# Performance work log

Hardware: AMD Instinct MI355X
Metric: run time of the kernel (lower is better)

## Reference

```python
import jax, jax.numpy as jnp
import numpy as np

N = 20000      # nodes
E1 = 100000    # topo (2d) edges
E2 = 100000    # distance edges
HID = 128      # hidden_size
N2D = 128      # node_embed_size_2d
E2D = 64       # edge_embed_size_2d
EF = 128       # edge_feat_size
ET = 32        # edge_type_size
NRBF = 64
CUT = 6.0


def rbf_expand(d):
    # Gaussian radial basis with cosine cutoff envelope, d: [E]
    centers = jnp.linspace(0.0, CUT, NRBF)
    width = CUT / NRBF
    env = 0.5 * (jnp.cos(jnp.pi * jnp.clip(d / CUT, 0.0, 1.0)) + 1.0)
    return jnp.exp(-((d[:, None] - centers) ** 2) / (2.0 * width * width)) * env[:, None]


def setup_inputs() -> dict:
    key = jax.random.key(0)
    ks = jax.random.split(key, 20)
    s = 0.02
    return {
        "H": jax.random.normal(ks[0], (N, HID), jnp.float32),
        "V": jax.random.normal(ks[1], (N, HID, 3), jnp.float32),
        "Z": jax.random.normal(ks[2], (N, 3), jnp.float32) * 3.0,
        "layer_i": 0,
        "H_2d": jax.random.normal(ks[3], (N, N2D), jnp.float32),
        "mask_2d": jnp.ones((N,), bool),
        "E2d_idx": jax.random.randint(ks[4], (2, E1), 0, N),
        "E2d_feat": jax.random.normal(ks[5], (E2D, E1), jnp.float32),
        "Z_3d": jax.random.normal(ks[6], (N, 3), jnp.float32) * 3.0,
        "mask_3d": jnp.ones((N,), bool),
        "Edist_idx": jax.random.randint(ks[7], (2, E2), 0, N),
        "Edist_val": jax.random.uniform(ks[8], (E2,), jnp.float32) * CUT,
        "virtual_node_embed": jax.random.normal(ks[9], (1, N2D), jnp.float32),
        "edge_type_embed": jax.random.normal(ks[10], (3, ET), jnp.float32),
        "W_rbf": jax.random.normal(ks[11], (EF, NRBF), jnp.float32) * s,
        "W_e2d": jax.random.normal(ks[12], (EF, E2D), jnp.float32) * s,
        "W_i": jax.random.normal(ks[13], (HID, HID + N2D), jnp.float32) * s,
        "W_phi1": jax.random.normal(ks[14], (HID, HID + EF + ET), jnp.float32) * s,
        "b_phi1": jnp.zeros((HID,), jnp.float32),
        "W_phi2": jax.random.normal(ks[15], (3 * HID, HID), jnp.float32) * s,
        "b_phi2": jnp.zeros((3 * HID,), jnp.float32),
        "W_msg": jax.random.normal(ks[16], (3 * HID, NRBF), jnp.float32) * s,
        "b_msg": jnp.zeros((3 * HID,), jnp.float32),
    }


def reference(H, V, Z, layer_i, H_2d, mask_2d, E2d_idx, E2d_feat, Z_3d, mask_3d,
              Edist_idx, Edist_val, virtual_node_embed, edge_type_embed,
              W_rbf, W_e2d, W_i, W_phi1, b_phi1, W_phi2, b_phi2, W_msg, b_msg):
    n = H.shape[0]
    # mask_3d is all-True in this fixture => n_cond_3d == n (static shapes)
    nodes_real = jnp.concatenate([H, H_2d], axis=-1)                       # [n, h1+h2]
    virt = jnp.broadcast_to(virtual_node_embed, (n, virtual_node_embed.shape[1]))
    nodes_virt = jnp.concatenate([H, virt], axis=-1)                        # [n, h1+h2]
    nodes = jnp.concatenate([nodes_real, nodes_virt], axis=0) @ W_i.T      # [2n, h1]
    v = jnp.concatenate([V, jnp.zeros_like(V)], axis=0)                     # [2n, h1, 3]
    z = jnp.concatenate([Z, Z_3d], axis=0)                                  # [2n, 3]

    row_3d = jnp.arange(n)
    col_3d = jnp.arange(n) + n
    E3d = jnp.stack([jnp.concatenate([row_3d, col_3d]),
                     jnp.concatenate([col_3d, row_3d])], axis=0)            # [2, 2n]
    edges = jnp.concatenate([E2d_idx, E3d, Edist_idx], axis=-1)             # [2, E]
    e1, e3, e2 = E2d_idx.shape[1], E3d.shape[1], Edist_idx.shape[1]
    edge_type = jnp.concatenate([jnp.zeros((e1,), jnp.int32),
                                 jnp.ones((e3,), jnp.int32),
                                 jnp.full((e2,), 2, jnp.int32)])
    et = edge_type_embed[edge_type]                                         # [E, ET]
    attr2d = E2d_feat.T @ W_e2d.T                                           # [e1, EF]
    attr3d = jnp.zeros((e3, W_e2d.shape[0]), jnp.float32)                   # [e3, EF]
    attrd = rbf_expand(Edist_val) @ W_rbf.T                                 # [e2, EF]
    edge_attr = jnp.concatenate(
        [jnp.concatenate([attr2d, attr3d, attrd], axis=0), et], axis=-1)    # [E, EF+ET]

    # AdapterLayer: PaiNN-style equivariant message passing
    row, col = edges[0], edges[1]
    rel = z[row] - z[col]                                                   # [E, 3]
    dist = jnp.sqrt(jnp.sum(rel * rel, axis=-1) + 1e-8)                     # [E]
    unit = rel / dist[:, None]
    phi_in = jnp.concatenate([nodes[col], edge_attr], axis=-1)
    phi = jax.nn.silu(phi_in @ W_phi1.T + b_phi1) @ W_phi2.T + b_phi2       # [E, 3h]
    wd = rbf_expand(dist) @ W_msg.T + b_msg                                 # [E, 3h]
    m = phi * wd
    h = nodes.shape[1]
    s_msg, v_gate, r_gate = m[:, :h], m[:, h:2 * h], m[:, 2 * h:]
    dv = v[col] * v_gate[:, :, None] + unit[:, None, :] * r_gate[:, :, None]  # [E, h, 3]
    nn2 = nodes.shape[0]
    H_add = jax.ops.segment_sum(s_msg, row, num_segments=nn2)[:n]
    V_add = jax.ops.segment_sum(dv, row, num_segments=nn2)[:n]

    # eval-mode clamp
    H_add = jnp.clip(H_add, -100.0, 100.0)
    V_add = jnp.clip(V_add, -100.0, 100.0)

    mask_dist = jnp.zeros((n,), bool).at[Edist_idx[0]].set(True).at[Edist_idx[1]].set(True)
    update_mask = mask_2d | mask_3d | mask_dist
    H_add = jnp.where(update_mask[:, None], H_add, 0.0)
    V_add = jnp.where(update_mask[:, None, None], V_add, 0.0)
    return H_add, V_add
```

## Files before the change

kernel.cpp:

```cpp
#include <hip/hip_runtime.h>
#include <hip/hip_bf16.h>

#define NN   20000
#define E1N  100000
#define E2N  100000
#define NEFF 220000
#define TILE 64
#define NBLK ((NEFF + TILE - 1) / TILE)
#define NPAD (NBLK * TILE)
#define RBF_STEP   0.09523809523809523f
#define RBF_INV2W2 56.88888888888889f

typedef short  bf16x8 __attribute__((ext_vector_type(8)));
typedef float  f32x4  __attribute__((ext_vector_type(4)));

__device__ __forceinline__ float4 ld4(const float* p) {
    return *reinterpret_cast<const float4*>(p);
}
__device__ __forceinline__ ushort f2bf(float x) {
    __hip_bfloat16 h = __float2bfloat16(x);
    return *reinterpret_cast<ushort*>(&h);
}
__device__ __forceinline__ float bf2f(ushort u) {
    return __uint_as_float(((unsigned)u) << 16);
}
__device__ __forceinline__ float env_of(float d) {
    float x = fminf(fmaxf(d * (1.0f / 6.0f), 0.0f), 1.0f);
    return 0.5f * (__cosf(3.14159265358979f * x) + 1.0f);
}
__device__ __forceinline__ float clip100(float x) {
    return fminf(fmaxf(x, -100.f), 100.f);
}

__device__ __forceinline__ int edge_row(int eid, const int* __restrict__ E2d_idx,
                                        const int* __restrict__ Edist_idx) {
    if (eid < E1N) return E2d_idx[eid];
    if (eid < E1N + NN) return eid - E1N;
    return Edist_idx[eid - E1N - NN];
}

__global__ __launch_bounds__(256) void hist_kernel(
    const int* __restrict__ E2d_idx, const int* __restrict__ Edist_idx,
    int* __restrict__ hist) {
    int g = blockIdx.x * 256 + threadIdx.x;
    if (g < NEFF) atomicAdd(&hist[edge_row(g, E2d_idx, Edist_idx)], 1);
}

__global__ __launch_bounds__(256) void scan_kernel(
    const int* __restrict__ hist, int* __restrict__ start, int* __restrict__ cursor) {
    __shared__ int wsum[4];
    const int t = threadIdx.x;
    const int base = t * 80;
    int s = 0;
    for (int j = 0; j < 80; ++j) {
        int idx = base + j;
        if (idx < NN) s += hist[idx];
    }
    const int lane = t & 63, w = t >> 6;
    int v = s;
    for (int off = 1; off < 64; off <<= 1) {
        int x = __shfl_up(v, off, 64);
        if (lane >= off) v += x;
    }
    if (lane == 63) wsum[w] = v;
    __syncthreads();
    int woff = 0;
    for (int i = 0; i < w; ++i) woff += wsum[i];
    int run = woff + v - s;
    for (int j = 0; j < 80; ++j) {
        int idx = base + j;
        if (idx < NN) {
            start[idx] = run;
            cursor[idx] = run;
            run += hist[idx];
        }
    }
    if (t == 255) start[NN] = run;
}

__global__ __launch_bounds__(256) void scatter_kernel(
    const int* __restrict__ E2d_idx, const int* __restrict__ Edist_idx,
    int* __restrict__ cursor, int* __restrict__ order) {
    int g = blockIdx.x * 256 + threadIdx.x;
    if (g < NEFF) {
        int r = edge_row(g, E2d_idx, Edist_idx);
        int pos = atomicAdd(&cursor[r], 1);
        order[pos] = g;
    }
}

__global__ __launch_bounds__(256) void meta_kernel(
    const int* __restrict__ order, const int* __restrict__ E2d_idx,
    const int* __restrict__ Edist_idx, const float* __restrict__ Edist_val,
    const float* __restrict__ Z, const float* __restrict__ Z3d,
    int4* __restrict__ metaI, float4* __restrict__ metaF,
    float4* __restrict__ metaU) {
    int g = blockIdx.x * 256 + threadIdx.x;
    if (g >= NPAD) return;
    int eid = (g < NEFF) ? order[g] : -1;
    int row, col, ty, e2 = 0; float dval = 0.f;
    if (eid < 0)             { ty = 1; row = -1; col = 0; }
    else if (eid < E1N)      { ty = 0; row = E2d_idx[eid]; col = E2d_idx[E1N + eid]; e2 = eid; }
    else if (eid < E1N + NN) { ty = 1; int jj = eid - E1N; row = jj; col = jj + NN; }
    else { ty = 2; int g2 = eid - E1N - NN;
           row = Edist_idx[g2]; col = Edist_idx[E2N + g2]; dval = Edist_val[g2]; }
    int rs = (row < 0) ? 0 : row;
    float prx = Z[rs * 3], pry = Z[rs * 3 + 1], prz = Z[rs * 3 + 2];
    float pcx, pcy, pcz;
    if (col < NN) { pcx = Z[col * 3]; pcy = Z[col * 3 + 1]; pcz = Z[col * 3 + 2]; }
    else { int c = col - NN; pcx = Z3d[c * 3]; pcy = Z3d[c * 3 + 1]; pcz = Z3d[c * 3 + 2]; }
    float dx = prx - pcx, dy = pry - pcy, dz = prz - pcz;
    float dist = sqrtf(dx * dx + dy * dy + dz * dz + 1e-8f);
    float inv = 1.0f / dist;
    int vcol = (col < NN) ? col : -1;
    metaI[g] = make_int4(col, row, ty, e2);
    metaF[g] = make_float4(dist, dval, env_of(dist), env_of(dval));
    metaU[g] = (row >= 0)
        ? make_float4(dx * inv, dy * inv, dz * inv, __int_as_float(vcol))
        : make_float4(0.f, 0.f, 0.f, __int_as_float(-1));
}

__global__ __launch_bounds__(256) void prep_kernel(
    const float* __restrict__ W_phi1, const float* __restrict__ b_phi1,
    const float* __restrict__ W_e2d, const float* __restrict__ W_rbf,
    const float* __restrict__ W_phi2, const float* __restrict__ W_msg,
    const float* __restrict__ et, const float* __restrict__ W_i,
    ushort* __restrict__ W1c, ushort* __restrict__ W2b,
    ushort* __restrict__ Wmb, float* __restrict__ b_type,
    ushort* __restrict__ Wib) {
    int g = blockIdx.x * 256 + threadIdx.x;
    if (g < 32768) {
        int n = g >> 8, k = g & 255;
        float v;
        if (k < 128) v = W_phi1[n * 288 + k];
        else {
            int kk = k - 128;
            const float* Wsel = (kk < 64) ? W_e2d : W_rbf;
            int j = kk & 63;
            float s = 0.f;
            for (int a = 0; a < 128; ++a) s += W_phi1[n * 288 + 128 + a] * Wsel[a * 64 + j];
            v = s;
        }
        W1c[n * 256 + k] = f2bf(v);
    } else if (g < 81920) {
        int q = g - 32768; W2b[q] = f2bf(W_phi2[q]);
    } else if (g < 106496) {
        int q = g - 81920; Wmb[q] = f2bf(W_msg[q]);
    } else if (g < 106880) {
        int q = g - 106496; int ty = q >> 7, n = q & 127;
        float s = b_phi1[n];
        for (int a = 0; a < 32; ++a) s += W_phi1[n * 288 + 256 + a] * et[ty * 32 + a];
        b_type[q] = s;
    } else if (g < 139648) {
        int q = g - 106880; Wib[q] = f2bf(W_i[q]);
    }
}

__global__ __launch_bounds__(256) void featT_kernel(
    const float* __restrict__ feat, ushort* __restrict__ featTb) {
    __shared__ float tile[64][65];
    const int t = threadIdx.x;
    const int cbase = blockIdx.x * 64;
    for (int i = t; i < 64 * 64; i += 256) {
        int k = i >> 6, e = i & 63;
        tile[k][e] = (cbase + e < E1N) ? feat[(size_t)k * E1N + cbase + e] : 0.f;
    }
    __syncthreads();
    for (int i = t; i < 64 * 64; i += 256) {
        int e = i >> 6, k = i & 63;
        if (cbase + e < E1N) featTb[(size_t)(cbase + e) * 64 + k] = f2bf(tile[k][e]);
    }
}

__global__ __launch_bounds__(256, 2) void nodes_mfma_kernel(
    const float* __restrict__ H, const float* __restrict__ H2d,
    const float* __restrict__ virt, const ushort* __restrict__ Wib,
    ushort* __restrict__ nodesb) {
    __shared__ ushort A[64][264];
    __shared__ ushort WB[128][132];

    const int t = threadIdx.x;
    const int gbase = blockIdx.x * 64;

    for (int i = t; i < 64 * 64; i += 256) {
        int e = i >> 6, q = i & 63;
        int row = gbase + e;
        float4 v;
        if (q < 32)          v = ld4(H + (size_t)((row < NN) ? row : row - NN) * 128 + q * 4);
        else if (row < NN)   v = ld4(H2d + (size_t)row * 128 + (q - 32) * 4);
        else                 v = ld4(virt + (q - 32) * 4);
        ushort tmp[4] = {f2bf(v.x), f2bf(v.y), f2bf(v.z), f2bf(v.w)};
        *reinterpret_cast<uint2*>(&A[e][q * 4]) = *reinterpret_cast<const uint2*>(tmp);
    }
    for (int i = t; i < 128 * 16; i += 256) {
        int n = i >> 4, q = i & 15;
        *reinterpret_cast<uint4*>(&WB[n][q * 8]) =
            *reinterpret_cast<const uint4*>(Wib + (size_t)n * 256 + q * 8);
    }
    __syncthreads();

    const int w  = t >> 6, lane = t & 63;
    const int mh = w >> 1, nh = w & 1;
    const int lr = lane >> 4, lc = lane & 15;
    const int ar0 = mh * 32 + lc;

    f32x4 acc[2][4];
#pragma unroll
    for (int mt = 0; mt < 2; ++mt)
#pragma unroll
        for (int nt = 0; nt < 4; ++nt) acc[mt][nt] = (f32x4){0.f, 0.f, 0.f, 0.f};
#pragma unroll
    for (int ks = 0; ks < 4; ++ks) {
        bf16x8 a0 = *reinterpret_cast<const bf16x8*>(&A[ar0][ks * 32 + lr * 8]);
        bf16x8 a1 = *reinterpret_cast<const bf16x8*>(&A[ar0 + 16][ks * 32 + lr * 8]);
#pragma unroll
        for (int nt = 0; nt < 4; ++nt) {
            int n = nh * 64 + nt * 16 + lc;
            bf16x8 b = *reinterpret_cast<const bf16x8*>(&WB[n][ks * 32 + lr * 8]);
            acc[0][nt] = __builtin_amdgcn_mfma_f32_16x16x32_bf16(a0, b, acc[0][nt], 0, 0, 0);
            acc[1][nt] = __builtin_amdgcn_mfma_f32_16x16x32_bf16(a1, b, acc[1][nt], 0, 0, 0);
        }
    }
    __syncthreads();
    for (int i = t; i < 128 * 16; i += 256) {
        int n = i >> 4, q = i & 15;
        *reinterpret_cast<uint4*>(&WB[n][q * 8]) =
            *reinterpret_cast<const uint4*>(Wib + (size_t)n * 256 + 128 + q * 8);
    }
    __syncthreads();
#pragma unroll
    for (int ks = 4; ks < 8; ++ks) {
        bf16x8 a0 = *reinterpret_cast<const bf16x8*>(&A[ar0][ks * 32 + lr * 8]);
        bf16x8 a1 = *reinterpret_cast<const bf16x8*>(&A[ar0 + 16][ks * 32 + lr * 8]);
#pragma unroll
        for (int nt = 0; nt < 4; ++nt) {
            int n = nh * 64 + nt * 16 + lc;
            bf16x8 b = *reinterpret_cast<const bf16x8*>(&WB[n][(ks - 4) * 32 + lr * 8]);
            acc[0][nt] = __builtin_amdgcn_mfma_f32_16x16x32_bf16(a0, b, acc[0][nt], 0, 0, 0);
            acc[1][nt] = __builtin_amdgcn_mfma_f32_16x16x32_bf16(a1, b, acc[1][nt], 0, 0, 0);
        }
    }
#pragma unroll
    for (int mt = 0; mt < 2; ++mt)
#pragma unroll
        for (int nt = 0; nt < 4; ++nt)
#pragma unroll
            for (int r = 0; r < 4; ++r) {
                int e  = mh * 32 + mt * 16 + lr * 4 + r;
                int ch = nh * 64 + nt * 16 + lc;
                nodesb[(size_t)(gbase + e) * 128 + ch] = f2bf(acc[mt][nt][r]);
            }
}

__global__ __launch_bounds__(256, 3) void edge1_kernel(
    const ushort* __restrict__ nodesb, const ushort* __restrict__ featTb,
    const ushort* __restrict__ W1c, const ushort* __restrict__ W2b,
    const ushort* __restrict__ Wmb, const float* __restrict__ b_type,
    const float* __restrict__ b_phi2, const float* __restrict__ b_msg,
    const int4* __restrict__ metaI, const float4* __restrict__ metaF,
    ushort* __restrict__ payloadM) {

    __shared__ ushort sm[26752];
    ushort* WB   = sm;
    ushort* HM   = sm + 16896;
    float*  s_bt = (float*)(sm + 25600);
    int*    s_col= (int*)(sm + 26368);
    int*    s_ty = (int*)(sm + 26496);
    int*    s_e2 = (int*)(sm + 26624);

    const int t = threadIdx.x;
    const int gbase = blockIdx.x * TILE;

    if (t < TILE) {
        int4 mi = metaI[gbase + t];
        s_col[t] = mi.x; s_ty[t] = mi.z; s_e2[t] = mi.w;
    }
    for (int i = t; i < 384; i += 256) s_bt[i] = b_type[i];
    for (int i = t; i < 128 * 16; i += 256) {
        int n = i >> 4, q = i & 15;
        *reinterpret_cast<uint4*>(WB + n * 132 + q * 8) =
            *reinterpret_cast<const uint4*>(W1c + (size_t)n * 256 + q * 8);
    }
    __syncthreads();

    const int w  = t >> 6, lane = t & 63;
    const int mh = w >> 1, nh = w & 1;
    const int lr = lane >> 4, lc = lane & 15;
    const int ar0 = mh * 32 + lc;

    const int colA = s_col[ar0],      colB = s_col[ar0 + 16];
    const int tyA  = s_ty[ar0],       tyB  = s_ty[ar0 + 16];
    const int e2A  = s_e2[ar0],       e2B  = s_e2[ar0 + 16];
    const float4 mfA = metaF[gbase + ar0];
    const float4 mfB = metaF[gbase + ar0 + 16];

    bf16x8 a0[8], a1[8];
    const bf16x8 zz = {0, 0, 0, 0, 0, 0, 0, 0};
#pragma unroll
    for (int ks = 0; ks < 4; ++ks) {
        a0[ks] = *reinterpret_cast<const bf16x8*>(nodesb + (size_t)colA * 128 + ks * 32 + lr * 8);
        a1[ks] = *reinterpret_cast<const bf16x8*>(nodesb + (size_t)colB * 128 + ks * 32 + lr * 8);
    }
#pragma unroll
    for (int ks = 4; ks < 6; ++ks) {
        bf16x8 fA = *reinterpret_cast<const bf16x8*>(featTb + (size_t)e2A * 64 + (ks - 4) * 32 + lr * 8);
        bf16x8 fB = *reinterpret_cast<const bf16x8*>(featTb + (size_t)e2B * 64 + (ks - 4) * 32 + lr * 8);
        a0[ks] = (tyA == 0) ? fA : zz;
        a1[ks] = (tyB == 0) ? fB : zz;
    }
#pragma unroll
    for (int ks = 6; ks < 8; ++ks) {
#pragma unroll
        for (int j = 0; j < 8; ++j) {
            float cc = (float)((ks - 6) * 32 + lr * 8 + j) * RBF_STEP;
            float tA = mfA.y - cc, tB = mfB.y - cc;
            ushort vA = f2bf(__expf(-tA * tA * RBF_INV2W2) * mfA.w);
            ushort vB = f2bf(__expf(-tB * tB * RBF_INV2W2) * mfB.w);
            a0[ks][j] = (tyA == 2) ? (short)vA : (short)0;
            a1[ks][j] = (tyB == 2) ? (short)vB : (short)0;
        }
    }
    bf16x8 ra0[2], ra1[2];
#pragma unroll
    for (int ks = 0; ks < 2; ++ks)
#pragma unroll
        for (int j = 0; j < 8; ++j) {
            float cc = (float)(ks * 32 + lr * 8 + j) * RBF_STEP;
            float tA = mfA.x - cc, tB = mfB.x - cc;
            ra0[ks][j] = (short)f2bf(__expf(-tA * tA * RBF_INV2W2) * mfA.z);
            ra1[ks][j] = (short)f2bf(__expf(-tB * tB * RBF_INV2W2) * mfB.z);
        }

    f32x4 acc[2][4];
#pragma unroll
    for (int mt = 0; mt < 2; ++mt)
#pragma unroll
        for (int nt = 0; nt < 4; ++nt) acc[mt][nt] = (f32x4){0.f, 0.f, 0.f, 0.f};
#pragma unroll
    for (int ks = 0; ks < 4; ++ks) {
#pragma unroll
        for (int nt = 0; nt < 4; ++nt) {
            int n = nh * 64 + nt * 16 + lc;
            bf16x8 b = *reinterpret_cast<const bf16x8*>(WB + n * 132 + ks * 32 + lr * 8);
            acc[0][nt] = __builtin_amdgcn_mfma_f32_16x16x32_bf16(a0[ks], b, acc[0][nt], 0, 0, 0);
            acc[1][nt] = __builtin_amdgcn_mfma_f32_16x16x32_bf16(a1[ks], b, acc[1][nt], 0, 0, 0);
        }
    }
    __syncthreads();
    for (int i = t; i < 128 * 16; i += 256) {
        int n = i >> 4, q = i & 15;
        *reinterpret_cast<uint4*>(WB + n * 132 + q * 8) =
            *reinterpret_cast<const uint4*>(W1c + (size_t)n * 256 + 128 + q * 8);
    }
    __syncthreads();
#pragma unroll
    for (int ks = 4; ks < 8; ++ks) {
#pragma unroll
        for (int nt = 0; nt < 4; ++nt) {
            int n = nh * 64 + nt * 16 + lc;
            bf16x8 b = *reinterpret_cast<const bf16x8*>(WB + n * 132 + (ks - 4) * 32 + lr * 8);
            acc[0][nt] = __builtin_amdgcn_mfma_f32_16x16x32_bf16(a0[ks], b, acc[0][nt], 0, 0, 0);
            acc[1][nt] = __builtin_amdgcn_mfma_f32_16x16x32_bf16(a1[ks], b, acc[1][nt], 0, 0, 0);
        }
    }
    __syncthreads();

#pragma unroll
    for (int mt = 0; mt < 2; ++mt)
#pragma unroll
        for (int nt = 0; nt < 4; ++nt)
#pragma unroll
            for (int r = 0; r < 4; ++r) {
                int e  = mh * 32 + mt * 16 + lr * 4 + r;
                int ch = nh * 64 + nt * 16 + lc;
                float x = acc[mt][nt][r] + s_bt[s_ty[e] * 128 + ch];
                HM[e * 136 + ch] = f2bf(x / (1.0f + __expf(-x)));
            }
    for (int i = t; i < 128 * 16; i += 256) {
        int n = i >> 4, q = i & 15;
        *reinterpret_cast<uint4*>(WB + n * 132 + q * 8) =
            *reinterpret_cast<const uint4*>(W2b + (size_t)n * 128 + q * 8);
    }
    __syncthreads();

    bf16x8 ha0[4], ha1[4];
#pragma unroll
    for (int ks = 0; ks < 4; ++ks) {
        ha0[ks] = *reinterpret_cast<const bf16x8*>(HM + ar0 * 136 + ks * 32 + lr * 8);
        ha1[ks] = *reinterpret_cast<const bf16x8*>(HM + (ar0 + 16) * 136 + ks * 32 + lr * 8);
    }

#pragma unroll
    for (int c = 0; c < 3; ++c) {
        f32x4 p[2][4], g[2][4];
#pragma unroll
        for (int mt = 0; mt < 2; ++mt)
#pragma unroll
            for (int nt = 0; nt < 4; ++nt) {
                p[mt][nt] = (f32x4){0.f, 0.f, 0.f, 0.f};
                g[mt][nt] = (f32x4){0.f, 0.f, 0.f, 0.f};
            }
#pragma unroll
        for (int ks = 0; ks < 4; ++ks) {
#pragma unroll
            for (int nt = 0; nt < 4; ++nt) {
                int n = nh * 64 + nt * 16 + lc;
                bf16x8 b = *reinterpret_cast<const bf16x8*>(WB + n * 132 + ks * 32 + lr * 8);
                p[0][nt] = __builtin_amdgcn_mfma_f32_16x16x32_bf16(ha0[ks], b, p[0][nt], 0, 0, 0);
                p[1][nt] = __builtin_amdgcn_mfma_f32_16x16x32_bf16(ha1[ks], b, p[1][nt], 0, 0, 0);
            }
        }
#pragma unroll
        for (int ks = 0; ks < 2; ++ks) {
#pragma unroll
            for (int nt = 0; nt < 4; ++nt) {
                int n = c * 128 + nh * 64 + nt * 16 + lc;
                bf16x8 b = *reinterpret_cast<const bf16x8*>(Wmb + (size_t)n * 64 + ks * 32 + lr * 8);
                g[0][nt] = __builtin_amdgcn_mfma_f32_16x16x32_bf16(ra0[ks], b, g[0][nt], 0, 0, 0);
                g[1][nt] = __builtin_amdgcn_mfma_f32_16x16x32_bf16(ra1[ks], b, g[1][nt], 0, 0, 0);
            }
        }
        __syncthreads();
#pragma unroll
        for (int mt = 0; mt < 2; ++mt)
#pragma unroll
            for (int nt = 0; nt < 4; ++nt) {
                int d  = nh * 64 + nt * 16 + lc;
                float b2 = b_phi2[c * 128 + d];
                float bm = b_msg[c * 128 + d];
#pragma unroll
                for (int r = 0; r < 4; ++r) {
                    int e = mh * 32 + mt * 16 + lr * 4 + r;
                    HM[e * 136 + d] = f2bf((p[mt][nt][r] + b2) * (g[mt][nt][r] + bm));
                }
            }
        if (c < 2) {
            for (int i = t; i < 128 * 16; i += 256) {
                int n = i >> 4, q = i & 15;
                *reinterpret_cast<uint4*>(WB + n * 132 + q * 8) =
                    *reinterpret_cast<const uint4*>(W2b + (size_t)((c + 1) * 128 + n) * 128 + q * 8);
            }
        }
        __syncthreads();
        for (int i = t; i < 2048; i += 256) {
            int e = i >> 5, q = i & 31;
            *reinterpret_cast<uint2*>(payloadM + (size_t)(gbase + e) * 384 + c * 128 + q * 4) =
                *reinterpret_cast<const uint2*>(HM + e * 136 + q * 4);
        }
    }
}

__global__ __launch_bounds__(256, 2) void edge0_kernel(
    const ushort* __restrict__ nodesb, const float* __restrict__ V,
    const float* __restrict__ Z, const float* __restrict__ Z3d,
    const int* __restrict__ E2d_idx, const float* __restrict__ E2d_feat,
    const int* __restrict__ Edist_idx, const float* __restrict__ Edist_val,
    const ushort* __restrict__ W1c, const ushort* __restrict__ W2b,
    const ushort* __restrict__ Wmb, const float* __restrict__ b_type,
    const float* __restrict__ b_phi2, const float* __restrict__ b_msg,
    float* __restrict__ Hout, float* __restrict__ Vout) {

    __shared__ ushort A1[TILE][264];
    __shared__ float  s_bt[3][128];
    __shared__ int    s_row[TILE], s_col[TILE], s_ty[TILE], s_e2[TILE], s_vcol[TILE];
    __shared__ float  s_dist[TILE], s_dval[TILE], s_env[TILE], s_env2[TILE];
    __shared__ float  s_unit[TILE][3];
    ushort (*hid)[136] = reinterpret_cast<ushort(*)[136]>(&A1[0][0]);

    const int t = threadIdx.x;
    const int gbase = blockIdx.x * TILE;
    if (t < TILE) {
        int gpos = gbase + t;
        int eid = (gpos < NEFF) ? gpos : -1;
        int row, col, ty, e2 = 0; float dval = 0.f;
        if (eid < 0)             { ty = 1; row = -1; col = 0; }
        else if (eid < E1N)      { ty = 0; row = E2d_idx[eid]; col = E2d_idx[E1N + eid]; e2 = eid; }
        else if (eid < E1N + NN) { ty = 1; int jj = eid - E1N; row = jj; col = jj + NN; }
        else { ty = 2; int g2 = eid - E1N - NN;
               row = Edist_idx[g2]; col = Edist_idx[E2N + g2]; dval = Edist_val[g2]; }
        int rs = (row < 0) ? 0 : row;
        float prx = Z[rs * 3], pry = Z[rs * 3 + 1], prz = Z[rs * 3 + 2];
        float pcx, pcy, pcz;
        if (col < NN) { pcx = Z[col * 3]; pcy = Z[col * 3 + 1]; pcz = Z[col * 3 + 2]; }
        else { int c = col - NN; pcx = Z3d[c * 3]; pcy = Z3d[c * 3 + 1]; pcz = Z3d[c * 3 + 2]; }
        float dx = prx - pcx, dy = pry - pcy, dz = prz - pcz;
        float dist = sqrtf(dx * dx + dy * dy + dz * dz + 1e-8f);
        float inv = 1.0f / dist;
        s_row[t] = row; s_col[t] = col; s_ty[t] = ty; s_e2[t] = e2;
        s_vcol[t] = (col < NN) ? col : -1;
        s_unit[t][0] = dx * inv; s_unit[t][1] = dy * inv; s_unit[t][2] = dz * inv;
        s_dist[t] = dist; s_dval[t] = dval;
        s_env[t] = env_of(dist); s_env2[t] = env_of(dval);
    }
    for (int i = t; i < 384; i += 256) ((float*)s_bt)[i] = b_type[i];
    __syncthreads();

    for (int i = t; i < TILE * 16; i += 256) {
        int e = i >> 4, q = i & 15;
        *reinterpret_cast<uint4*>(&A1[e][q * 8]) =
            *reinterpret_cast<const uint4*>(nodesb + (size_t)s_col[e] * 128 + q * 8);
    }
    for (int i = t; i < TILE * 128; i += 256) {
        int k = i >> 6, e = i & 63;
        int ty = s_ty[e];
        float v = 0.f;
        if (ty == 0) { if (k < 64) v = E2d_feat[(size_t)k * E1N + s_e2[e]]; }
        else if (ty == 2) {
            if (k >= 64) {
                float dd = s_dval[e] - (float)(k - 64) * RBF_STEP;
                v = __expf(-dd * dd * RBF_INV2W2) * s_env2[e];
            }
        }
        A1[e][128 + k] = f2bf(v);
    }
    __syncthreads();

    const int w  = t >> 6, lane = t & 63;
    const int mh = w >> 1, nh = w & 1;
    const int lr = lane >> 4, lc = lane & 15;
    const int ar0 = mh * 32 + lc;

    bf16x8 ra0[2], ra1[2];
    {
        float dA = s_dist[ar0],      eA = s_env[ar0];
        float dB = s_dist[ar0 + 16], eB = s_env[ar0 + 16];
#pragma unroll
        for (int ks = 0; ks < 2; ++ks)
#pragma unroll
            for (int j = 0; j < 8; ++j) {
                float c  = (float)(ks * 32 + lr * 8 + j) * RBF_STEP;
                float tA = dA - c, tB = dB - c;
                ra0[ks][j] = (short)f2bf(__expf(-tA * tA * RBF_INV2W2) * eA);
                ra1[ks][j] = (short)f2bf(__expf(-tB * tB * RBF_INV2W2) * eB);
            }
    }

    f32x4 acc[2][4];
#pragma unroll
    for (int mt = 0; mt < 2; ++mt)
#pragma unroll
        for (int nt = 0; nt < 4; ++nt) acc[mt][nt] = (f32x4){0.f, 0.f, 0.f, 0.f};
#pragma unroll
    for (int ks = 0; ks < 8; ++ks) {
        bf16x8 a0 = *reinterpret_cast<const bf16x8*>(&A1[ar0][ks * 32 + lr * 8]);
        bf16x8 a1 = *reinterpret_cast<const bf16x8*>(&A1[ar0 + 16][ks * 32 + lr * 8]);
#pragma unroll
        for (int nt = 0; nt < 4; ++nt) {
            int n = nh * 64 + nt * 16 + lc;
            bf16x8 b = *reinterpret_cast<const bf16x8*>(W1c + (size_t)n * 256 + ks * 32 + lr * 8);
            acc[0][nt] = __builtin_amdgcn_mfma_f32_16x16x32_bf16(a0, b, acc[0][nt], 0, 0, 0);
            acc[1][nt] = __builtin_amdgcn_mfma_f32_16x16x32_bf16(a1, b, acc[1][nt], 0, 0, 0);
        }
    }
    __syncthreads();
#pragma unroll
    for (int mt = 0; mt < 2; ++mt)
#pragma unroll
        for (int nt = 0; nt < 4; ++nt)
#pragma unroll
            for (int r = 0; r < 4; ++r) {
                int e  = mh * 32 + mt * 16 + lr * 4 + r;
                int ch = nh * 64 + nt * 16 + lc;
                float x = acc[mt][nt][r] + s_bt[s_ty[e]][ch];
                hid[e][ch] = f2bf(x / (1.0f + __expf(-x)));
            }
    __syncthreads();

    f32x4 vgr[2][4];
#pragma unroll
    for (int c = 0; c < 3; ++c) {
        f32x4 p[2][4], g[2][4];
#pragma unroll
        for (int mt = 0; mt < 2; ++mt)
#pragma unroll
            for (int nt = 0; nt < 4; ++nt) {
                p[mt][nt] = (f32x4){0.f, 0.f, 0.f, 0.f};
                g[mt][nt] = (f32x4){0.f, 0.f, 0.f, 0.f};
            }
#pragma unroll
        for (int ks = 0; ks < 4; ++ks) {
            bf16x8 a0 = *reinterpret_cast<const bf16x8*>(&hid[ar0][ks * 32 + lr * 8]);
            bf16x8 a1 = *reinterpret_cast<const bf16x8*>(&hid[ar0 + 16][ks * 32 + lr * 8]);
#pragma unroll
            for (int nt = 0; nt < 4; ++nt) {
                int n = c * 128 + nh * 64 + nt * 16 + lc;
                bf16x8 b = *reinterpret_cast<const bf16x8*>(W2b + (size_t)n * 128 + ks * 32 + lr * 8);
                p[0][nt] = __builtin_amdgcn_mfma_f32_16x16x32_bf16(a0, b, p[0][nt], 0, 0, 0);
                p[1][nt] = __builtin_amdgcn_mfma_f32_16x16x32_bf16(a1, b, p[1][nt], 0, 0, 0);
            }
        }
#pragma unroll
        for (int ks = 0; ks < 2; ++ks) {
#pragma unroll
            for (int nt = 0; nt < 4; ++nt) {
                int n = c * 128 + nh * 64 + nt * 16 + lc;
                bf16x8 b = *reinterpret_cast<const bf16x8*>(Wmb + (size_t)n * 64 + ks * 32 + lr * 8);
                g[0][nt] = __builtin_amdgcn_mfma_f32_16x16x32_bf16(ra0[ks], b, g[0][nt], 0, 0, 0);
                g[1][nt] = __builtin_amdgcn_mfma_f32_16x16x32_bf16(ra1[ks], b, g[1][nt], 0, 0, 0);
            }
        }
#pragma unroll
        for (int mt = 0; mt < 2; ++mt)
#pragma unroll
            for (int nt = 0; nt < 4; ++nt) {
                int d  = nh * 64 + nt * 16 + lc;
                float b2 = b_phi2[c * 128 + d];
                float bm = b_msg[c * 128 + d];
#pragma unroll
                for (int r = 0; r < 4; ++r) {
                    int e = mh * 32 + mt * 16 + lr * 4 + r;
                    float m = (p[mt][nt][r] + b2) * (g[mt][nt][r] + bm);
                    int row = s_row[e];
                    if (c == 0) {
                        if (row >= 0) unsafeAtomicAdd(&Hout[(size_t)row * 128 + d], m);
                    } else if (c == 1) {
                        vgr[mt][nt][r] = m;
                    } else if (row >= 0) {
                        float vgv = vgr[mt][nt][r];
                        int vc = s_vcol[e];
                        float vx = 0.f, vy = 0.f, vz = 0.f;
                        if (vc >= 0) {
                            const float* vp = V + ((size_t)vc * 128 + d) * 3;
                            vx = vp[0]; vy = vp[1]; vz = vp[2];
                        }
                        float* vo = Vout + ((size_t)row * 128 + d) * 3;
                        unsafeAtomicAdd(vo + 0, vx * vgv + s_unit[e][0] * m);
                        unsafeAtomicAdd(vo + 1, vy * vgv + s_unit[e][1] * m);
                        unsafeAtomicAdd(vo + 2, vz * vgv + s_unit[e][2] * m);
                    }
                }
            }
    }
}

__global__ __launch_bounds__(256) void reduce_kernel(
    const ushort* __restrict__ payloadM, const float4* __restrict__ metaU,
    const float* __restrict__ V, const int* __restrict__ start,
    float* __restrict__ Hout, float* __restrict__ Vout) {
    const int t = threadIdx.x;
    const int rbase = blockIdx.x * 8;
    const bool hside = (t < 128);
    const int d = hside ? t : (t - 128);
    for (int nr = 0; nr < 8; ++nr) {
        int r = rbase + nr;
        if (r >= NN) return;
        int a = start[r], b = start[r + 1];
        int n = b - a;
        if (hside) {
            const ushort* base = payloadM + (size_t)a * 384 + d;
            float a0 = 0.f, a1 = 0.f, a2 = 0.f, a3 = 0.f;
            int i = 0;
            for (; i + 4 <= n; i += 4) {
                a0 += bf2f(base[(size_t)i * 384]);
                a1 += bf2f(base[(size_t)(i + 1) * 384]);
                a2 += bf2f(base[(size_t)(i + 2) * 384]);
                a3 += bf2f(base[(size_t)(i + 3) * 384]);
            }
            for (; i < n; ++i) a0 += bf2f(base[(size_t)i * 384]);
            Hout[(size_t)r * 128 + d] = clip100((a0 + a1) + (a2 + a3));
        } else {
            const ushort* base = payloadM + (size_t)a * 384;
            const float4* ub = metaU + a;
            float ax = 0.f, ay = 0.f, az = 0.f;
            float bx = 0.f, by = 0.f, bz = 0.f;
            int i = 0;
            for (; i + 2 <= n; i += 2) {
                const ushort* pm0 = base + (size_t)i * 384;
                const ushort* pm1 = base + (size_t)(i + 1) * 384;
                float vg0 = bf2f(pm0[128 + d]), rg0 = bf2f(pm0[256 + d]);
                float vg1 = bf2f(pm1[128 + d]), rg1 = bf2f(pm1[256 + d]);
                float4 u0 = ub[i];
                float4 u1 = ub[i + 1];
                int vc0 = __float_as_int(u0.w);
                int vc1 = __float_as_int(u1.w);
                if (vc0 >= 0) {
                    const float* vp = V + (size_t)vc0 * 384 + d * 3;
                    ax += vg0 * vp[0]; ay += vg0 * vp[1]; az += vg0 * vp[2];
                }
                if (vc1 >= 0) {
                    const float* vp = V + (size_t)vc1 * 384 + d * 3;
                    bx += vg1 * vp[0]; by += vg1 * vp[1]; bz += vg1 * vp[2];
                }
                ax += rg0 * u0.x; ay += rg0 * u0.y; az += rg0 * u0.z;
                bx += rg1 * u1.x; by += rg1 * u1.y; bz += rg1 * u1.z;
            }
            if (i < n) {
                const ushort* pm0 = base + (size_t)i * 384;
                float vg0 = bf2f(pm0[128 + d]), rg0 = bf2f(pm0[256 + d]);
                float4 u0 = ub[i];
                int vc0 = __float_as_int(u0.w);
                if (vc0 >= 0) {
                    const float* vp = V + (size_t)vc0 * 384 + d * 3;
                    ax += vg0 * vp[0]; ay += vg0 * vp[1]; az += vg0 * vp[2];
                }
                ax += rg0 * u0.x; ay += rg0 * u0.y; az += rg0 * u0.z;
            }
            float* vo = Vout + (size_t)r * 384 + d * 3;
            vo[0] = clip100(ax + bx);
            vo[1] = clip100(ay + by);
            vo[2] = clip100(az + bz);
        }
    }
}

extern "C" void kernel_launch(void* const* d_in, const int* in_sizes, int n_in,
                              void* d_out, int out_size, void* d_ws, size_t ws_size,
                              hipStream_t stream) {
    const float* H         = (const float*)d_in[0];
    const float* V         = (const float*)d_in[1];
    const float* Z         = (const float*)d_in[2];
    const float* H2d       = (const float*)d_in[4];
    const int*   E2d_idx   = (const int*)d_in[6];
    const float* E2d_feat  = (const float*)d_in[7];
    const float* Z3d       = (const float*)d_in[8];
    const int*   Edist_idx = (const int*)d_in[10];
    const float* Edist_val = (const float*)d_in[11];
    const float* virt      = (const float*)d_in[12];
    const float* et        = (const float*)d_in[13];
    const float* W_rbf     = (const float*)d_in[14];
    const float* W_e2d     = (const float*)d_in[15];
    const float* W_i       = (const float*)d_in[16];
    const float* W_phi1    = (const float*)d_in[17];
    const float* b_phi1    = (const float*)d_in[18];
    const float* W_phi2    = (const float*)d_in[19];
    const float* b_phi2    = (const float*)d_in[20];
    const float* W_msg     = (const float*)d_in[21];
    const float* b_msg     = (const float*)d_in[22];

    ushort* nodesb  = (ushort*)d_ws;
    ushort* W1c     = nodesb + 5120000;
    ushort* W2b     = W1c + 32768;
    ushort* Wmb     = W2b + 49152;
    ushort* Wib     = Wmb + 24576;
    float*  b_type  = (float*)(Wib + 32768);
    ushort* featTb  = (ushort*)(b_type + 384);
    int*    hist    = (int*)(featTb + (size_t)E1N * 64);
    int*    cursor  = hist + NN;
    int*    start   = cursor + NN;
    int*    order   = start + NN + 1;
    int4*   metaI   = (int4*)(((size_t)(order + NPAD) + 15) & ~(size_t)15);
    float4* metaF   = (float4*)(metaI + NPAD);
    float4* metaU   = metaF + NPAD;

    size_t fixed = (size_t)((char*)(metaU + NPAD) - (char*)d_ws);
    size_t poff  = (fixed + 255) & ~(size_t)255;
    size_t need  = poff + (size_t)NPAD * 384 * sizeof(ushort);
    const bool big = (ws_size >= need);
    ushort* payloadM = (ushort*)((char*)d_ws + poff);

    float* Hout = (float*)d_out;
    float* Vout = Hout + (size_t)NN * 128;

    prep_kernel<<<(139648 + 255) / 256, 256, 0, stream>>>(
        W_phi1, b_phi1, W_e2d, W_rbf, W_phi2, W_msg, et, W_i,
        W1c, W2b, Wmb, b_type, Wib);
    nodes_mfma_kernel<<<(2 * NN) / 64, 256, 0, stream>>>(H, H2d, virt, Wib, nodesb);

    if (big) {
        hipMemsetAsync(hist, 0, NN * sizeof(int), stream);
        featT_kernel<<<(E1N + 63) / 64, 256, 0, stream>>>(E2d_feat, featTb);
        hist_kernel<<<(NEFF + 255) / 256, 256, 0, stream>>>(E2d_idx, Edist_idx, hist);
        scan_kernel<<<1, 256, 0, stream>>>(hist, start, cursor);
        scatter_kernel<<<(NEFF + 255) / 256, 256, 0, stream>>>(E2d_idx, Edist_idx, cursor, order);
        meta_kernel<<<(NPAD + 255) / 256, 256, 0, stream>>>(
            order, E2d_idx, Edist_idx, Edist_val, Z, Z3d, metaI, metaF, metaU);
        edge1_kernel<<<NBLK, 256, 0, stream>>>(
            nodesb, featTb, W1c, W2b, Wmb, b_type, b_phi2, b_msg,
            metaI, metaF, payloadM);
        reduce_kernel<<<(NN + 7) / 8, 256, 0, stream>>>(
            payloadM, metaU, V, start, Hout, Vout);
    } else {
        hipMemsetAsync(d_out, 0, (size_t)out_size * sizeof(float), stream);
        edge0_kernel<<<NBLK, 256, 0, stream>>>(
            nodesb, V, Z, Z3d, E2d_idx, E2d_feat, Edist_idx, Edist_val,
            W1c, W2b, Wmb, b_type, b_phi2, b_msg, Hout, Vout);
    }
}
```

Measured before the change: 443.7 us.

## Stage edge MLP A-operand in LDS and unroll reduce loop deeper

The first-layer A operand (gathered node features, edge features, distance RBF) is now built cooperatively in shared memory with coalesced row loads, instead of each lane keeping eight bf16x8 register fragments filled by scattered per-lane gathers. This lowers register pressure, and the occupancy hint drops from 3 to 2 blocks because LDS use per block grows. Separately, the reduce kernel handles 4 rows per block instead of 8 and unrolls the V accumulation by 4 to expose more memory-level parallelism. The cost is extra LDS traffic and barriers, plus a lower occupancy target for edge1.

```diff
diff --git a/kernel.cpp b/kernel.cpp
--- a/kernel.cpp
+++ b/kernel.cpp
@@ -252,7 +252,7 @@
             }
 }
 
-__global__ __launch_bounds__(256, 3) void edge1_kernel(
+__global__ __launch_bounds__(256, 2) void edge1_kernel(
     const ushort* __restrict__ nodesb, const ushort* __restrict__ featTb,
     const ushort* __restrict__ W1c, const ushort* __restrict__ W2b,
     const ushort* __restrict__ Wmb, const float* __restrict__ b_type,
@@ -260,13 +260,14 @@
     const int4* __restrict__ metaI, const float4* __restrict__ metaF,
     ushort* __restrict__ payloadM) {
 
-    __shared__ ushort sm[26752];
-    ushort* WB   = sm;
-    ushort* HM   = sm + 16896;
-    float*  s_bt = (float*)(sm + 25600);
-    int*    s_col= (int*)(sm + 26368);
-    int*    s_ty = (int*)(sm + 26496);
-    int*    s_e2 = (int*)(sm + 26624);
+    __shared__ ushort A1f[TILE * 264 + 256];
+    __shared__ ushort WB[128][132];
+    __shared__ float  s_bt[3][128];
+    __shared__ int    s_col[TILE], s_ty[TILE], s_e2[TILE];
+    __shared__ float  s_dval[TILE], s_env2[TILE];
+
+    ushort* hidp  = A1f;
+    ushort* m_lds = A1f + 8704;
 
     const int t = threadIdx.x;
     const int gbase = blockIdx.x * TILE;
@@ -274,11 +275,33 @@
     if (t < TILE) {
         int4 mi = metaI[gbase + t];
         s_col[t] = mi.x; s_ty[t] = mi.z; s_e2[t] = mi.w;
-    }
-    for (int i = t; i < 384; i += 256) s_bt[i] = b_type[i];
+        float4 mf = metaF[gbase + t];
+        s_dval[t] = mf.y; s_env2[t] = mf.w;
+    }
+    for (int i = t; i < 384; i += 256) ((float*)s_bt)[i] = b_type[i];
+    __syncthreads();
+
+    for (int i = t; i < TILE * 16; i += 256) {
+        int e = i >> 4, q = i & 15;
+        *reinterpret_cast<uint4*>(&A1f[e * 264 + q * 8]) =
+            *reinterpret_cast<const uint4*>(nodesb + (size_t)s_col[e] * 128 + q * 8);
+    }
+    for (int i = t; i < TILE * 128; i += 256) {
+        int e = i >> 7, k = i & 127;
+        int ty = s_ty[e];
+        ushort v = 0;
+        if (ty == 0) { if (k < 64) v = featTb[(size_t)s_e2[e] * 64 + k]; }
+        else if (ty == 2) {
+            if (k >= 64) {
+                float dd = s_dval[e] - (float)(k - 64) * RBF_STEP;
+                v = f2bf(__expf(-dd * dd * RBF_INV2W2) * s_env2[e]);
+            }
+        }
+        A1f[e * 264 + 128 + k] = v;
+    }
     for (int i = t; i < 128 * 16; i += 256) {
         int n = i >> 4, q = i & 15;
-        *reinterpret_cast<uint4*>(WB + n * 132 + q * 8) =
+        *reinterpret_cast<uint4*>(&WB[n][q * 8]) =
             *reinterpret_cast<const uint4*>(W1c + (size_t)n * 256 + q * 8);
     }
     __syncthreads();
@@ -288,38 +311,8 @@
     const int lr = lane >> 4, lc = lane & 15;
     const int ar0 = mh * 32 + lc;
 
-    const int colA = s_col[ar0],      colB = s_col[ar0 + 16];
-    const int tyA  = s_ty[ar0],       tyB  = s_ty[ar0 + 16];
-    const int e2A  = s_e2[ar0],       e2B  = s_e2[ar0 + 16];
     const float4 mfA = metaF[gbase + ar0];
     const float4 mfB = metaF[gbase + ar0 + 16];
-
-    bf16x8 a0[8], a1[8];
-    const bf16x8 zz = {0, 0, 0, 0, 0, 0, 0, 0};
-#pragma unroll
-    for (int ks = 0; ks < 4; ++ks) {
-        a0[ks] = *reinterpret_cast<const bf16x8*>(nodesb + (size_t)colA * 128 + ks * 32 + lr * 8);
-        a1[ks] = *reinterpret_cast<const bf16x8*>(nodesb + (size_t)colB * 128 + ks * 32 + lr * 8);
-    }
-#pragma unroll
-    for (int ks = 4; ks < 6; ++ks) {
-        bf16x8 fA = *reinterpret_cast<const bf16x8*>(featTb + (size_t)e2A * 64 + (ks - 4) * 32 + lr * 8);
-        bf16x8 fB = *reinterpret_cast<const bf16x8*>(featTb + (size_t)e2B * 64 + (ks - 4) * 32 + lr * 8);
-        a0[ks] = (tyA == 0) ? fA : zz;
-        a1[ks] = (tyB == 0) ? fB : zz;
-    }
-#pragma unroll
-    for (int ks = 6; ks < 8; ++ks) {
-#pragma unroll
-        for (int j = 0; j < 8; ++j) {
-            float cc = (float)((ks - 6) * 32 + lr * 8 + j) * RBF_STEP;
-            float tA = mfA.y - cc, tB = mfB.y - cc;
-            ushort vA = f2bf(__expf(-tA * tA * RBF_INV2W2) * mfA.w);
-            ushort vB = f2bf(__expf(-tB * tB * RBF_INV2W2) * mfB.w);
-            a0[ks][j] = (tyA == 2) ? (short)vA : (short)0;
-            a1[ks][j] = (tyB == 2) ? (short)vB : (short)0;
-        }
-    }
     bf16x8 ra0[2], ra1[2];
 #pragma unroll
     for (int ks = 0; ks < 2; ++ks)
@@ -338,29 +331,33 @@
         for (int nt = 0; nt < 4; ++nt) acc[mt][nt] = (f32x4){0.f, 0.f, 0.f, 0.f};
 #pragma unroll
     for (int ks = 0; ks < 4; ++ks) {
+        bf16x8 a0 = *reinterpret_cast<const bf16x8*>(&A1f[ar0 * 264 + ks * 32 + lr * 8]);
+        bf16x8 a1 = *reinterpret_cast<const bf16x8*>(&A1f[(ar0 + 16) * 264 + ks * 32 + lr * 8]);
 #pragma unroll
         for (int nt = 0; nt < 4; ++nt) {
             int n = nh * 64 + nt * 16 + lc;
-            bf16x8 b = *reinterpret_cast<const bf16x8*>(WB + n * 132 + ks * 32 + lr * 8);
-            acc[0][nt] = __builtin_amdgcn_mfma_f32_16x16x32_bf16(a0[ks], b, acc[0][nt], 0, 0, 0);
-            acc[1][nt] = __builtin_amdgcn_mfma_f32_16x16x32_bf16(a1[ks], b, acc[1][nt], 0, 0, 0);
+            bf16x8 b = *reinterpret_cast<const bf16x8*>(&WB[n][ks * 32 + lr * 8]);
+            acc[0][nt] = __builtin_amdgcn_mfma_f32_16x16x32_bf16(a0, b, acc[0][nt], 0, 0, 0);
+            acc[1][nt] = __builtin_amdgcn_mfma_f32_16x16x32_bf16(a1, b, acc[1][nt], 0, 0, 0);
         }
     }
     __syncthreads();
     for (int i = t; i < 128 * 16; i += 256) {
         int n = i >> 4, q = i & 15;
-        *reinterpret_cast<uint4*>(WB + n * 132 + q * 8) =
+        *reinterpret_cast<uint4*>(&WB[n][q * 8]) =
             *reinterpret_cast<const uint4*>(W1c + (size_t)n * 256 + 128 + q * 8);
     }
     __syncthreads();
 #pragma unroll
     for (int ks = 4; ks < 8; ++ks) {
+        bf16x8 a0 = *reinterpret_cast<const bf16x8*>(&A1f[ar0 * 264 + ks * 32 + lr * 8]);
+        bf16x8 a1 = *reinterpret_cast<const bf16x8*>(&A1f[(ar0 + 16) * 264 + ks * 32 + lr * 8]);
 #pragma unroll
         for (int nt = 0; nt < 4; ++nt) {
             int n = nh * 64 + nt * 16 + lc;
-            bf16x8 b = *reinterpret_cast<const bf16x8*>(WB + n * 132 + (ks - 4) * 32 + lr * 8);
-            acc[0][nt] = __builtin_amdgcn_mfma_f32_16x16x32_bf16(a0[ks], b, acc[0][nt], 0, 0, 0);
-            acc[1][nt] = __builtin_amdgcn_mfma_f32_16x16x32_bf16(a1[ks], b, acc[1][nt], 0, 0, 0);
+            bf16x8 b = *reinterpret_cast<const bf16x8*>(&WB[n][(ks - 4) * 32 + lr * 8]);
+            acc[0][nt] = __builtin_amdgcn_mfma_f32_16x16x32_bf16(a0, b, acc[0][nt], 0, 0, 0);
+            acc[1][nt] = __builtin_amdgcn_mfma_f32_16x16x32_bf16(a1, b, acc[1][nt], 0, 0, 0);
         }
     }
     __syncthreads();
@@ -373,12 +370,12 @@
             for (int r = 0; r < 4; ++r) {
                 int e  = mh * 32 + mt * 16 + lr * 4 + r;
                 int ch = nh * 64 + nt * 16 + lc;
-                float x = acc[mt][nt][r] + s_bt[s_ty[e] * 128 + ch];
-                HM[e * 136 + ch] = f2bf(x / (1.0f + __expf(-x)));
+                float x = acc[mt][nt][r] + s_bt[s_ty[e]][ch];
+                hidp[e * 136 + ch] = f2bf(x / (1.0f + __expf(-x)));
             }
     for (int i = t; i < 128 * 16; i += 256) {
         int n = i >> 4, q = i & 15;
-        *reinterpret_cast<uint4*>(WB + n * 132 + q * 8) =
+        *reinterpret_cast<uint4*>(&WB[n][q * 8]) =
             *reinterpret_cast<const uint4*>(W2b + (size_t)n * 128 + q * 8);
     }
     __syncthreads();
@@ -386,8 +383,8 @@
     bf16x8 ha0[4], ha1[4];
 #pragma unroll
     for (int ks = 0; ks < 4; ++ks) {
-        ha0[ks] = *reinterpret_cast<const bf16x8*>(HM + ar0 * 136 + ks * 32 + lr * 8);
-        ha1[ks] = *reinterpret_cast<const bf16x8*>(HM + (ar0 + 16) * 136 + ks * 32 + lr * 8);
+        ha0[ks] = *reinterpret_cast<const bf16x8*>(&hidp[ar0 * 136 + ks * 32 + lr * 8]);
+        ha1[ks] = *reinterpret_cast<const bf16x8*>(&hidp[(ar0 + 16) * 136 + ks * 32 + lr * 8]);
     }
 
 #pragma unroll
@@ -405,7 +402,7 @@
 #pragma unroll
             for (int nt = 0; nt < 4; ++nt) {
                 int n = nh * 64 + nt * 16 + lc;
-                bf16x8 b = *reinterpret_cast<const bf16x8*>(WB + n * 132 + ks * 32 + lr * 8);
+                bf16x8 b = *reinterpret_cast<const bf16x8*>(&WB[n][ks * 32 + lr * 8]);
                 p[0][nt] = __builtin_amdgcn_mfma_f32_16x16x32_bf16(ha0[ks], b, p[0][nt], 0, 0, 0);
                 p[1][nt] = __builtin_amdgcn_mfma_f32_16x16x32_bf16(ha1[ks], b, p[1][nt], 0, 0, 0);
             }
@@ -431,13 +428,13 @@
 #pragma unroll
                 for (int r = 0; r < 4; ++r) {
                     int e = mh * 32 + mt * 16 + lr * 4 + r;
-                    HM[e * 136 + d] = f2bf((p[mt][nt][r] + b2) * (g[mt][nt][r] + bm));
+                    m_lds[e * 132 + d] = f2bf((p[mt][nt][r] + b2) * (g[mt][nt][r] + bm));
                 }
             }
         if (c < 2) {
             for (int i = t; i < 128 * 16; i += 256) {
                 int n = i >> 4, q = i & 15;
-                *reinterpret_cast<uint4*>(WB + n * 132 + q * 8) =
+                *reinterpret_cast<uint4*>(&WB[n][q * 8]) =
                     *reinterpret_cast<const uint4*>(W2b + (size_t)((c + 1) * 128 + n) * 128 + q * 8);
             }
         }
@@ -445,7 +442,7 @@
         for (int i = t; i < 2048; i += 256) {
             int e = i >> 5, q = i & 31;
             *reinterpret_cast<uint2*>(payloadM + (size_t)(gbase + e) * 384 + c * 128 + q * 4) =
-                *reinterpret_cast<const uint2*>(HM + e * 136 + q * 4);
+                *reinterpret_cast<const uint2*>(m_lds + e * 132 + q * 4);
         }
     }
 }
@@ -638,10 +635,10 @@
     const float* __restrict__ V, const int* __restrict__ start,
     float* __restrict__ Hout, float* __restrict__ Vout) {
     const int t = threadIdx.x;
-    const int rbase = blockIdx.x * 8;
+    const int rbase = blockIdx.x * 4;
     const bool hside = (t < 128);
     const int d = hside ? t : (t - 128);
-    for (int nr = 0; nr < 8; ++nr) {
+    for (int nr = 0; nr < 4; ++nr) {
         int r = rbase + nr;
         if (r >= NN) return;
         int a = start[r], b = start[r + 1];
@@ -664,15 +661,20 @@
             float ax = 0.f, ay = 0.f, az = 0.f;
             float bx = 0.f, by = 0.f, bz = 0.f;
             int i = 0;
-            for (; i + 2 <= n; i += 2) {
+            for (; i + 4 <= n; i += 4) {
                 const ushort* pm0 = base + (size_t)i * 384;
                 const ushort* pm1 = base + (size_t)(i + 1) * 384;
+                const ushort* pm2 = base + (size_t)(i + 2) * 384;
+                const ushort* pm3 = base + (size_t)(i + 3) * 384;
                 float vg0 = bf2f(pm0[128 + d]), rg0 = bf2f(pm0[256 + d]);
                 float vg1 = bf2f(pm1[128 + d]), rg1 = bf2f(pm1[256 + d]);
-                float4 u0 = ub[i];
-                float4 u1 = ub[i + 1];
+                float vg2 = bf2f(pm2[128 + d]), rg2 = bf2f(pm2[256 + d]);
+                float vg3 = bf2f(pm3[128 + d]), rg3 = bf2f(pm3[256 + d]);
+                float4 u0 = ub[i], u1 = ub[i + 1], u2 = ub[i + 2], u3 = ub[i + 3];
                 int vc0 = __float_as_int(u0.w);
                 int vc1 = __float_as_int(u1.w);
+                int vc2 = __float_as_int(u2.w);
+                int vc3 = __float_as_int(u3.w);
                 if (vc0 >= 0) {
                     const float* vp = V + (size_t)vc0 * 384 + d * 3;
                     ax += vg0 * vp[0]; ay += vg0 * vp[1]; az += vg0 * vp[2];
@@ -681,10 +683,20 @@
                     const float* vp = V + (size_t)vc1 * 384 + d * 3;
                     bx += vg1 * vp[0]; by += vg1 * vp[1]; bz += vg1 * vp[2];
                 }
+                if (vc2 >= 0) {
+                    const float* vp = V + (size_t)vc2 * 384 + d * 3;
+                    ax += vg2 * vp[0]; ay += vg2 * vp[1]; az += vg2 * vp[2];
+                }
+                if (vc3 >= 0) {
+                    const float* vp = V + (size_t)vc3 * 384 + d * 3;
+                    bx += vg3 * vp[0]; by += vg3 * vp[1]; bz += vg3 * vp[2];
+                }
                 ax += rg0 * u0.x; ay += rg0 * u0.y; az += rg0 * u0.z;
                 bx += rg1 * u1.x; by += rg1 * u1.y; bz += rg1 * u1.z;
-            }
-            if (i < n) {
+                ax += rg2 * u2.x; ay += rg2 * u2.y; az += rg2 * u2.z;
+                bx += rg3 * u3.x; by += rg3 * u3.y; bz += rg3 * u3.z;
+            }
+            for (; i < n; ++i) {
                 const ushort* pm0 = base + (size_t)i * 384;
                 float vg0 = bf2f(pm0[128 + d]), rg0 = bf2f(pm0[256 + d]);
                 float4 u0 = ub[i];
@@ -767,7 +779,7 @@
         edge1_kernel<<<NBLK, 256, 0, stream>>>(
             nodesb, featTb, W1c, W2b, Wmb, b_type, b_phi2, b_msg,
             metaI, metaF, payloadM);
-        reduce_kernel<<<(NN + 7) / 8, 256, 0, stream>>>(
+        reduce_kernel<<<(NN + 3) / 4, 256, 0, stream>>>(
             payloadM, metaU, V, start, Hout, Vout);
     } else {
         hipMemsetAsync(d_out, 0, (size_t)out_size * sizeof(float), stream);
```

After: 399.5 us, median of 2. -10.0%, faster.
